# Kernel optimization log

Measured on AMD Instinct MI355X. Metric: run time of the kernel, lower is better.

The kernel has to match this reference:

```python
import jax, jax.numpy as jnp
import numpy as np

USER_NUM = 100000
ITEM_NUM = 100000  # padding index; table has ITEM_NUM+1 rows
D = 64
B = 4096
L = 200
NEG_WEIGHT = 0.1


def setup_inputs() -> dict:
    key = jax.random.key(0)
    k1, k2, k3, k4, k5 = jax.random.split(key, 5)
    uids = jax.random.randint(k1, (B,), 0, USER_NUM, dtype=jnp.int64 if jax.config.jax_enable_x64 else jnp.int32)
    pos_iids = jax.random.randint(k2, (B, L), 0, ITEM_NUM + 1, dtype=jnp.int64 if jax.config.jax_enable_x64 else jnp.int32)
    user_W = jax.random.normal(k3, (USER_NUM, D), dtype=jnp.float32) * 0.1
    item_W = jax.random.normal(k4, (ITEM_NUM + 1, D), dtype=jnp.float32) * 0.1
    h = jnp.full((D, 1), 0.01, dtype=jnp.float32)  # reset_para: constant 0.01
    return {"uids": uids, "pos_iids": pos_iids, "user_W": user_W, "item_W": item_W, "h": h}


def reference(uids, pos_iids, user_W, item_W, h):
    u_emb = user_W[uids]                      # [B, D] (dropout p=0 -> identity)
    pos_embs = item_W[pos_iids]               # [B, L, D]
    mask = (pos_iids != ITEM_NUM).astype(u_emb.dtype)  # padding id masked out
    pos_embs = pos_embs * mask[:, :, None]
    # hpq[b,l] = sum_d u[b,d] * pos[b,l,d] * h[d]
    hpq = jnp.einsum('bd,bld,d->bl', u_emb, pos_embs, h[:, 0])
    pos_data_loss = jnp.sum((1.0 - NEG_WEIGHT) * jnp.square(hpq) - 2.0 * hpq)
    # part_1/part_2 in torch are sums of per-row outer products == Gram matrices
    part_1 = item_W.T @ item_W                # [D, D]
    part_2 = u_emb.T @ u_emb                  # [D, D]
    part_3 = h @ h.T                          # [D, D]
    all_data_loss = jnp.sum(part_1 * part_2 * part_3)
    return NEG_WEIGHT * all_data_loss + pos_data_loss
```

## Files before the change

kernel.cpp:

```cpp
#include <hip/hip_runtime.h>

#define D 64
#define ITEM_PAD 100000
#define LSEQ 200
#define BATCH 4096
#define NEG_W 0.1f
#define NBI 512
#define NBU 64
#define GSZ (D * D)
#define PITEM_OFF 0
#define PUSER_OFF ((size_t)NBI * GSZ)
#define POS_OFF   (PUSER_OFF + (size_t)NBU * GSZ)
#define WS2_OFF   (POS_OFF + BATCH)
#define WS_FLOATS (WS2_OFF + 256)

__global__ void fused_partials(const int* __restrict__ uids,
                               const int* __restrict__ pos_iids,
                               const float* __restrict__ user_W,
                               const float* __restrict__ item_W,
                               const float* __restrict__ h,
                               float* __restrict__ ws) {
    __shared__ float smem[16 * D];
    const int bid = blockIdx.x;
    const int t   = threadIdx.x;

    if (bid < NBI + NBU) {
        const bool item = (bid < NBI);
        const float* __restrict__ W = item ? item_W : user_W;
        const int* __restrict__ idx = item ? nullptr : uids;
        const int nrows   = item ? (ITEM_PAD + 1) : BATCH;
        const int stride  = item ? NBI : NBU;
        const int b0      = item ? bid : bid - NBI;
        float* __restrict__ out =
            ws + (item ? PITEM_OFF + (size_t)b0 * GSZ : PUSER_OFF + (size_t)b0 * GSZ);

        const int ti = t >> 4;
        const int tj = t & 15;
        float acc[4][4] = {{0.f,0.f,0.f,0.f},{0.f,0.f,0.f,0.f},
                           {0.f,0.f,0.f,0.f},{0.f,0.f,0.f,0.f}};

        const int nchunks = (nrows + 15) >> 4;
        for (int c = b0; c < nchunks; c += stride) {
            const int r = (c << 4) + ti;
            float4 v = make_float4(0.f, 0.f, 0.f, 0.f);
            if (r < nrows) {
                const int src = idx ? idx[r] : r;
                v = *(const float4*)(W + (size_t)src * D + tj * 4);
            }
            __syncthreads();
            *(float4*)(smem + ti * D + tj * 4) = v;
            __syncthreads();

            #pragma unroll
            for (int r2 = 0; r2 < 16; ++r2) {
                float xi[4], xj[4];
                *(float4*)xi = *(const float4*)(smem + r2 * D + ti * 4);
                *(float4*)xj = *(const float4*)(smem + r2 * D + tj * 4);
                #pragma unroll
                for (int a = 0; a < 4; ++a)
                    #pragma unroll
                    for (int b2 = 0; b2 < 4; ++b2)
                        acc[a][b2] += xi[a] * xj[b2];
            }
        }
        #pragma unroll
        for (int a = 0; a < 4; ++a)
            *(float4*)(out + (ti * 4 + a) * D + tj * 4) = *(const float4*)acc[a];
    } else {
        const int b = bid - (NBI + NBU);
        float* uh  = smem;
        int*   sidx = (int*)(smem + D);
        float* red = smem + D + LSEQ;

        if (t < LSEQ) sidx[t] = pos_iids[(size_t)b * LSEQ + t];
        if (t >= 192) {
            const int j = t - 192;
            uh[j] = user_W[(size_t)uids[b] * D + j] * h[j];
        }
        __syncthreads();

        const int lane = t & 63;
        const int wave = t >> 6;
        const int p    = lane >> 4;
        const int q    = lane & 15;
        const int base = wave * 4 + p;

        const float4 u4 = *(const float4*)(uh + q * 4);

        int ids[13];
        #pragma unroll
        for (int k = 0; k < 13; ++k) {
            const int l = base + 16 * k;
            ids[k] = (l < LSEQ) ? sidx[l] : ITEM_PAD;
        }
        float4 rows[13];
        #pragma unroll
        for (int k = 0; k < 13; ++k) {
            float4 v = make_float4(0.f, 0.f, 0.f, 0.f);
            if (ids[k] != ITEM_PAD)
                v = *(const float4*)(item_W + (size_t)ids[k] * D + q * 4);
            rows[k] = v;
        }

        float local = 0.f;
        #pragma unroll
        for (int k = 0; k < 13; ++k) {
            float s = u4.x*rows[k].x + u4.y*rows[k].y + u4.z*rows[k].z + u4.w*rows[k].w;
            s += __shfl_xor(s, 1);
            s += __shfl_xor(s, 2);
            s += __shfl_xor(s, 4);
            s += __shfl_xor(s, 8);
            if (q == 0)
                local += (1.0f - NEG_W) * s * s - 2.0f * s;
        }
        local += __shfl_xor(local, 1);
        local += __shfl_xor(local, 2);
        local += __shfl_xor(local, 4);
        local += __shfl_xor(local, 8);
        local += __shfl_xor(local, 16);
        local += __shfl_xor(local, 32);
        if (lane == 0) red[wave] = local;
        __syncthreads();
        if (t == 0)
            ws[POS_OFF + b] = red[0] + red[1] + red[2] + red[3];
    }
}

__global__ void reduce_partials(const float* __restrict__ ws,
                                const float* __restrict__ h,
                                float* __restrict__ ws2) {
    __shared__ float rI[4][16];
    __shared__ float rU[4][16];
    const int b  = blockIdx.x;
    const int t  = threadIdx.x;
    const int kk = t & 15;
    const int ps = t >> 4;
    const int lane = t & 63;
    const int wave = t >> 6;
    const int k  = b * 16 + kk;

    float si = 0.f, su = 0.f;
    #pragma unroll 8
    for (int p = ps; p < NBI; p += 16) si += ws[PITEM_OFF + (size_t)p * GSZ + k];
    #pragma unroll
    for (int p = ps; p < NBU; p += 16) su += ws[PUSER_OFF + (size_t)p * GSZ + k];

    si += __shfl_xor(si, 16); si += __shfl_xor(si, 32);
    su += __shfl_xor(su, 16); su += __shfl_xor(su, 32);
    if (lane < 16) { rI[wave][kk] = si; rU[wave][kk] = su; }
    __syncthreads();

    float c = 0.f;
    if (t < 16) {
        const float Gi = rI[0][t] + rI[1][t] + rI[2][t] + rI[3][t];
        const float Gu = rU[0][t] + rU[1][t] + rU[2][t] + rU[3][t];
        const int kg = b * 16 + t;
        const int i = kg >> 6, j = kg & 63;
        c = NEG_W * Gi * Gu * h[i] * h[j] + ws[POS_OFF + b * 16 + t];
    }
    if (wave == 0) {
        c += __shfl_xor(c, 1);
        c += __shfl_xor(c, 2);
        c += __shfl_xor(c, 4);
        c += __shfl_xor(c, 8);
        if (lane == 0) ws2[b] = c;
    }
}

__global__ void final_sum(const float* __restrict__ ws2, float* __restrict__ out) {
    __shared__ float red[4];
    const int t = threadIdx.x;
    float s = ws2[t];
    s += __shfl_xor(s, 1);
    s += __shfl_xor(s, 2);
    s += __shfl_xor(s, 4);
    s += __shfl_xor(s, 8);
    s += __shfl_xor(s, 16);
    s += __shfl_xor(s, 32);
    const int lane = t & 63, wave = t >> 6;
    if (lane == 0) red[wave] = s;
    __syncthreads();
    if (t == 0) out[0] = red[0] + red[1] + red[2] + red[3];
}

extern "C" void kernel_launch(void* const* d_in, const int* in_sizes, int n_in,
                              void* d_out, int out_size, void* d_ws, size_t ws_size,
                              hipStream_t stream) {
    const int*   uids     = (const int*)d_in[0];
    const int*   pos_iids = (const int*)d_in[1];
    const float* user_W   = (const float*)d_in[2];
    const float* item_W   = (const float*)d_in[3];
    const float* h        = (const float*)d_in[4];
    float* out = (float*)d_out;
    float* ws  = (float*)d_ws;

    fused_partials<<<NBI + NBU + BATCH, 256, 0, stream>>>(uids, pos_iids, user_W,
                                                          item_W, h, ws);
    reduce_partials<<<256, 256, 0, stream>>>(ws, h, ws + WS2_OFF);
    final_sum<<<1, 256, 0, stream>>>(ws + WS2_OFF, out);
}
```

Measured before the change: 126.3 us.

## Prefetch next Gram chunk into registers and fuse final reduction via atomic counter

The Gram-matrix blocks now load 32 rows per iteration and issue the global loads for the next chunk before computing on the current one, overlapping memory latency with FMA work. The separate final_sum kernel is removed: the reduce kernel increments a global counter, and the last block to arrive sums the per-block partials, saving one launch. The counter is reset inside the first kernel. This adds more shared memory and registers per block, and relies on threadfence and atomic ordering for correctness.

```diff
diff --git a/kernel.cpp b/kernel.cpp
--- a/kernel.cpp
+++ b/kernel.cpp
@@ -12,7 +12,7 @@
 #define PUSER_OFF ((size_t)NBI * GSZ)
 #define POS_OFF   (PUSER_OFF + (size_t)NBU * GSZ)
 #define WS2_OFF   (POS_OFF + BATCH)
-#define WS_FLOATS (WS2_OFF + 256)
+#define CTR_OFF   (WS2_OFF + 256)
 
 __global__ void fused_partials(const int* __restrict__ uids,
                                const int* __restrict__ pos_iids,
@@ -20,17 +20,19 @@
                                const float* __restrict__ item_W,
                                const float* __restrict__ h,
                                float* __restrict__ ws) {
-    __shared__ float smem[16 * D];
+    __shared__ float smem[32 * D];
     const int bid = blockIdx.x;
     const int t   = threadIdx.x;
+
+    if (bid == 0 && t == 0) ((unsigned*)(ws + CTR_OFF))[0] = 0u;
 
     if (bid < NBI + NBU) {
         const bool item = (bid < NBI);
         const float* __restrict__ W = item ? item_W : user_W;
         const int* __restrict__ idx = item ? nullptr : uids;
-        const int nrows   = item ? (ITEM_PAD + 1) : BATCH;
-        const int stride  = item ? NBI : NBU;
-        const int b0      = item ? bid : bid - NBI;
+        const int nrows  = item ? (ITEM_PAD + 1) : BATCH;
+        const int stride = item ? NBI : NBU;
+        const int b0     = item ? bid : bid - NBI;
         float* __restrict__ out =
             ws + (item ? PITEM_OFF + (size_t)b0 * GSZ : PUSER_OFF + (size_t)b0 * GSZ);
 
@@ -39,20 +41,44 @@
         float acc[4][4] = {{0.f,0.f,0.f,0.f},{0.f,0.f,0.f,0.f},
                            {0.f,0.f,0.f,0.f},{0.f,0.f,0.f,0.f}};
 
-        const int nchunks = (nrows + 15) >> 4;
-        for (int c = b0; c < nchunks; c += stride) {
-            const int r = (c << 4) + ti;
-            float4 v = make_float4(0.f, 0.f, 0.f, 0.f);
-            if (r < nrows) {
-                const int src = idx ? idx[r] : r;
-                v = *(const float4*)(W + (size_t)src * D + tj * 4);
-            }
+        const int nchunks = (nrows + 31) >> 5;
+
+        float4 va = make_float4(0.f,0.f,0.f,0.f), vb = va;
+        int c = b0;
+        if (c < nchunks) {
+            const int ra = (c << 5) + ti, rb = ra + 16;
+            if (ra < nrows) {
+                const int sa = idx ? idx[ra] : ra;
+                va = *(const float4*)(W + (size_t)sa * D + tj * 4);
+            }
+            if (rb < nrows) {
+                const int sb = idx ? idx[rb] : rb;
+                vb = *(const float4*)(W + (size_t)sb * D + tj * 4);
+            }
+        }
+
+        for (; c < nchunks; ) {
             __syncthreads();
-            *(float4*)(smem + ti * D + tj * 4) = v;
+            *(float4*)(smem + ti * D + tj * 4)        = va;
+            *(float4*)(smem + (ti + 16) * D + tj * 4) = vb;
             __syncthreads();
 
+            const int cn = c + stride;
+            va = make_float4(0.f,0.f,0.f,0.f); vb = va;
+            if (cn < nchunks) {
+                const int ra = (cn << 5) + ti, rb = ra + 16;
+                if (ra < nrows) {
+                    const int sa = idx ? idx[ra] : ra;
+                    va = *(const float4*)(W + (size_t)sa * D + tj * 4);
+                }
+                if (rb < nrows) {
+                    const int sb = idx ? idx[rb] : rb;
+                    vb = *(const float4*)(W + (size_t)sb * D + tj * 4);
+                }
+            }
+
             #pragma unroll
-            for (int r2 = 0; r2 < 16; ++r2) {
+            for (int r2 = 0; r2 < 32; ++r2) {
                 float xi[4], xj[4];
                 *(float4*)xi = *(const float4*)(smem + r2 * D + ti * 4);
                 *(float4*)xj = *(const float4*)(smem + r2 * D + tj * 4);
@@ -62,15 +88,16 @@
                     for (int b2 = 0; b2 < 4; ++b2)
                         acc[a][b2] += xi[a] * xj[b2];
             }
+            c = cn;
         }
         #pragma unroll
         for (int a = 0; a < 4; ++a)
             *(float4*)(out + (ti * 4 + a) * D + tj * 4) = *(const float4*)acc[a];
     } else {
         const int b = bid - (NBI + NBU);
-        float* uh  = smem;
+        float* uh   = smem;
         int*   sidx = (int*)(smem + D);
-        float* red = smem + D + LSEQ;
+        float* red  = smem + D + LSEQ;
 
         if (t < LSEQ) sidx[t] = pos_iids[(size_t)b * LSEQ + t];
         if (t >= 192) {
@@ -126,11 +153,14 @@
     }
 }
 
-__global__ void reduce_partials(const float* __restrict__ ws,
-                                const float* __restrict__ h,
-                                float* __restrict__ ws2) {
+__global__ void reduce_final(const float* __restrict__ ws,
+                             const float* __restrict__ h,
+                             float* __restrict__ ws2,
+                             unsigned* __restrict__ counter,
+                             float* __restrict__ out) {
     __shared__ float rI[4][16];
     __shared__ float rU[4][16];
+    __shared__ int isLast;
     const int b  = blockIdx.x;
     const int t  = threadIdx.x;
     const int kk = t & 15;
@@ -165,22 +195,27 @@
         c += __shfl_xor(c, 8);
         if (lane == 0) ws2[b] = c;
     }
-}
-
-__global__ void final_sum(const float* __restrict__ ws2, float* __restrict__ out) {
-    __shared__ float red[4];
-    const int t = threadIdx.x;
-    float s = ws2[t];
-    s += __shfl_xor(s, 1);
-    s += __shfl_xor(s, 2);
-    s += __shfl_xor(s, 4);
-    s += __shfl_xor(s, 8);
-    s += __shfl_xor(s, 16);
-    s += __shfl_xor(s, 32);
-    const int lane = t & 63, wave = t >> 6;
-    if (lane == 0) red[wave] = s;
+
+    if (t == 0) {
+        __threadfence();
+        const unsigned old = atomicAdd(counter, 1u);
+        isLast = (old == 255u);
+    }
     __syncthreads();
-    if (t == 0) out[0] = red[0] + red[1] + red[2] + red[3];
+    if (isLast) {
+        __threadfence();
+        float s = ws2[t];
+        s += __shfl_xor(s, 1);
+        s += __shfl_xor(s, 2);
+        s += __shfl_xor(s, 4);
+        s += __shfl_xor(s, 8);
+        s += __shfl_xor(s, 16);
+        s += __shfl_xor(s, 32);
+        __shared__ float red[4];
+        if (lane == 0) red[wave] = s;
+        __syncthreads();
+        if (t == 0) out[0] = red[0] + red[1] + red[2] + red[3];
+    }
 }
 
 extern "C" void kernel_launch(void* const* d_in, const int* in_sizes, int n_in,
@@ -196,6 +231,6 @@
 
     fused_partials<<<NBI + NBU + BATCH, 256, 0, stream>>>(uids, pos_iids, user_W,
                                                           item_W, h, ws);
-    reduce_partials<<<256, 256, 0, stream>>>(ws, h, ws + WS2_OFF);
-    final_sum<<<1, 256, 0, stream>>>(ws + WS2_OFF, out);
+    reduce_final<<<256, 256, 0, stream>>>(ws, h, ws + WS2_OFF,
+                                          (unsigned*)(ws + CTR_OFF), out);
 }
```

New measurement: 130.8 us. +3.6%, slower.
